# Kernel optimization log

Hardware: AMD Instinct MI355X
Metric: run time of the kernel (lower is better)

The kernel has to match this reference:

```python
import jax, jax.numpy as jnp
import numpy as np
from jax import lax

R = 0.1  # radius_graph radius (matches init kwarg r)


def setup_inputs() -> dict:
    key = jax.random.key(0)
    ks = jax.random.split(key, 16)
    B, O, K, F = 8, 4, 512, 3
    H = 128
    def lin(k, fan_in, fan_out):
        return jax.random.normal(k, (fan_in, fan_out), jnp.float32) / np.sqrt(fan_in)
    return {
        "points": jax.random.uniform(ks[0], (B, O, K, F), jnp.float32),
        "com": jax.random.normal(ks[1], (B, O, 3), jnp.float32),
        "com_vel": jax.random.normal(ks[2], (B, O, 3), jnp.float32),
        "angle": jax.random.normal(ks[3], (B, O, 3), jnp.float32),
        "angle_vel": jax.random.normal(ks[4], (B, O, 3), jnp.float32),
        "padding": jnp.ones((B, O, K), jnp.float32),
        "W0": lin(ks[5], 2 * F, H), "b0": jnp.zeros((H,), jnp.float32),
        "W1": lin(ks[6], H, H), "b1": jnp.zeros((H,), jnp.float32),
        "W2": lin(ks[7], H, H), "b2": jnp.zeros((H,), jnp.float32),
        "Wfc": lin(ks[8], H, 2 * F), "bfc": jnp.zeros((2 * F,), jnp.float32),
        "knn": 8,
        "pred_len": 10,
    }


def reference(points, com, com_vel, angle, angle_vel, padding,
              W0, b0, W1, b1, W2, b2, Wfc, bfc, knn, pred_len):
    B, O, K, F = points.shape
    N = O * K  # nodes per batch element
    pad = padding.reshape(B, N)                       # float mask [B,N]
    padb = pad > 0
    edge_ok = padb[:, :, None] & padb[:, None, :]     # valid src & dst
    not_self = ~jnp.eye(N, dtype=bool)
    eye = jnp.eye(N, dtype=points.dtype)

    states0 = jnp.concatenate([points, jnp.zeros_like(points)], -1).reshape(B, N, 2 * F)

    def gconv(a_hat, dinv, x, W, b):
        # GCNConv: out_i = sum_j A_hat[ij] d_i^-1/2 d_j^-1/2 (xW)_j + b
        h = (x @ W) * dinv[..., None]
        return jnp.einsum('bij,bjd->bid', a_hat, h) * dinv[..., None] + b

    def step(states, _):
        pos = states[..., :3]                         # [B,N,3]
        d2 = jnp.sum((pos[:, :, None, :] - pos[:, None, :, :]) ** 2, -1)
        adj = (d2 < R * R) & not_self & edge_ok       # radius_graph + padding mask
        a_hat = lax.stop_gradient(adj.astype(states.dtype) + eye)  # self-loops (all nodes)
        dinv = lax.rsqrt(a_hat.sum(-1))               # deg >= 1
        x = jax.nn.relu(gconv(a_hat, dinv, states, W0, b0))
        x = jax.nn.relu(gconv(a_hat, dinv, x, W1, b1))
        x = jax.nn.relu(gconv(a_hat, dinv, x, W2, b2))
        res = x @ Wfc + bfc
        new = states + res * pad[..., None]
        return new, new

    _, traj = lax.scan(step, states0, None, length=pred_len)
    traj = jnp.concatenate([states0[:, None], jnp.swapaxes(traj, 0, 1)], axis=1)
    return traj.reshape(B, pred_len + 1, O, K, 2 * F)[..., :3]
```

## Files before the change

### kernel.cpp

```cpp
#include <hip/hip_runtime.h>
#include <math.h>

#define BB 8
#define NN 2048
#define HH 128
#define NSEG 8
#define SEGJ 256
#define SEGCAP 12
#define MAXNBR (NSEG*SEGCAP)
#define PREDL 10
#define TSTRIDE (NN*3)
#define OUT_BSTRIDE ((PREDL+1)*NN*3)


__global__ __launch_bounds__(256) void k_init(const float* __restrict__ points,
                                              float* __restrict__ states,
                                              float* __restrict__ out) {
    int idx = blockIdx.x * 256 + threadIdx.x;
    if (idx >= BB * NN) return;
    int b = idx >> 11;
    int n = idx & 2047;
    float px = points[idx * 3 + 0];
    float py = points[idx * 3 + 1];
    float pz = points[idx * 3 + 2];
    float* s = states + (size_t)idx * 6;
    s[0] = px; s[1] = py; s[2] = pz; s[3] = 0.f; s[4] = 0.f; s[5] = 0.f;
    float* o = out + (size_t)b * OUT_BSTRIDE + n * 3;
    o[0] = px; o[1] = py; o[2] = pz;
}

__global__ __launch_bounds__(512, 2) void k_adj(const float* __restrict__ states,
                                                float* __restrict__ xs0,
                                                float* __restrict__ dinv,
                                                int* __restrict__ nbr,
                                                int* __restrict__ cntN) {
    const float R2c = 0.01f;
    int b = blockIdx.x & 7;
    int tile = blockIdx.x >> 3;
    __shared__ float4 pos[NN];
    __shared__ int degs[512];
    __shared__ unsigned short jb[512][SEGCAP];
    const float* sb = states + (size_t)b * NN * 6;
    for (int j = threadIdx.x; j < NN; j += 512) {
        const float* r = sb + j * 6;
        pos[j] = make_float4(r[0], r[1], r[2], 0.f);
    }
    __syncthreads();
    int node = threadIdx.x & 63;
    int seg  = threadIdx.x >> 6;
    int i = tile * 64 + node;
    int gi = b * NN + i;
    float4 pi = pos[i];
    int cnt = 0;
    int j0 = seg * SEGJ;
#pragma unroll 4
    for (int j = j0; j < j0 + SEGJ; ++j) {
        float4 pj = pos[j];
        float dx = pi.x - pj.x;
        float dy = pi.y - pj.y;
        float dz = pi.z - pj.z;
        float d2 = __fadd_rn(__fadd_rn(__fmul_rn(dx, dx), __fmul_rn(dy, dy)),
                             __fmul_rn(dz, dz));
        if (d2 < R2c && j != i) {
            if (cnt < SEGCAP) jb[threadIdx.x][cnt] = (unsigned short)j;
            cnt++;
        }
    }
    if (cnt > SEGCAP) cnt = SEGCAP;
    degs[threadIdx.x] = cnt;
    __syncthreads();
    int off = 0;
    for (int s = 0; s < seg; ++s) off += degs[s * 64 + node];
    int base = gi * MAXNBR + off;
    for (int k = 0; k < cnt; ++k) nbr[base + k] = (int)jb[threadIdx.x][k];
    if (seg == NSEG - 1) {
        int tot = off + cnt;
        cntN[gi] = tot;
        float di = (float)(1.0 / sqrt((double)(1 + tot)));
        dinv[gi] = di;
        const float* srow = sb + (size_t)i * 6;
        float* xr = xs0 + (size_t)gi * 6;
#pragma unroll
        for (int c = 0; c < 6; ++c) xr[c] = di * srow[c];
    }
}

__global__ __launch_bounds__(512, 4) void k_l0(const float* __restrict__ xs0,
                                               const float* __restrict__ dinv,
                                               const int* __restrict__ nbr,
                                               const int* __restrict__ cntN,
                                               const float* __restrict__ W0,
                                               const float* __restrict__ b0,
                                               float* __restrict__ xs1) {
    int b = blockIdx.x & 7;
    int tile = blockIdx.x >> 3;
    int node = threadIdx.x >> 4;
    int part = threadIdx.x & 15;
    int i = tile * 32 + node;
    int gi = b * NN + i;
    float g[6];
    {
        const float* sr = xs0 + (size_t)gi * 6;
        float2 a0 = *(const float2*)sr;
        float2 a1 = *(const float2*)(sr + 2);
        float2 a2 = *(const float2*)(sr + 4);
        g[0] = a0.x; g[1] = a0.y; g[2] = a1.x; g[3] = a1.y; g[4] = a2.x; g[5] = a2.y;
    }
    int cnt = cntN[gi];
    const int* nb = nbr + gi * MAXNBR;
    for (int k = 0; k < cnt; ++k) {
        int j = nb[k];
        const float* xr = xs0 + (size_t)(b * NN + j) * 6;
        float2 v0 = *(const float2*)xr;
        float2 v1 = *(const float2*)(xr + 2);
        float2 v2 = *(const float2*)(xr + 4);
        g[0] += v0.x; g[1] += v0.y; g[2] += v1.x;
        g[3] += v1.y; g[4] += v2.x; g[5] += v2.y;
    }
    float di = dinv[gi];
#pragma unroll
    for (int c = 0; c < 6; ++c) g[c] *= di;
    int c0 = part * 8;
    float y[8];
#pragma unroll
    for (int r = 0; r < 2; ++r) {
        float4 bv = *(const float4*)(b0 + c0 + r * 4);
        y[r * 4 + 0] = bv.x; y[r * 4 + 1] = bv.y; y[r * 4 + 2] = bv.z; y[r * 4 + 3] = bv.w;
    }
#pragma unroll
    for (int k = 0; k < 6; ++k) {
        float u = g[k];
        const float* wr = W0 + k * HH + c0;
#pragma unroll
        for (int r = 0; r < 2; ++r) {
            float4 w = *(const float4*)(wr + r * 4);
            y[r * 4 + 0] = fmaf(u, w.x, y[r * 4 + 0]);
            y[r * 4 + 1] = fmaf(u, w.y, y[r * 4 + 1]);
            y[r * 4 + 2] = fmaf(u, w.z, y[r * 4 + 2]);
            y[r * 4 + 3] = fmaf(u, w.w, y[r * 4 + 3]);
        }
    }
    float* xo = xs1 + (size_t)gi * HH + c0;
#pragma unroll
    for (int r = 0; r < 2; ++r) {
        float4 v;
        v.x = di * fmaxf(y[r * 4 + 0], 0.f);
        v.y = di * fmaxf(y[r * 4 + 1], 0.f);
        v.z = di * fmaxf(y[r * 4 + 2], 0.f);
        v.w = di * fmaxf(y[r * 4 + 3], 0.f);
        *(float4*)(xo + r * 4) = v;
    }
}

__device__ __forceinline__ void gather_into_lds(const float* __restrict__ xin,
                                                const float* __restrict__ dinv,
                                                const int* __restrict__ nbr,
                                                const int* __restrict__ cntN,
                                                int b, int tile,
                                                float (*uS)[HH + 4]) {
    const int node = threadIdx.x >> 4;
    const int part = threadIdx.x & 15;
    const int i = tile * 32 + node;
    const int gi = b * NN + i;
    const int c0 = part * 8;
    float acc[8];
    const float* xs = xin + (size_t)gi * HH + c0;
#pragma unroll
    for (int r = 0; r < 2; ++r) *(float4*)&acc[r * 4] = *(const float4*)(xs + r * 4);
    const int cnt = cntN[gi];
    const int* nb = nbr + gi * MAXNBR;
    for (int k = 0; k < cnt; ++k) {
        const int j = nb[k];
        const float* xr = xin + (size_t)(b * NN + j) * HH + c0;
#pragma unroll
        for (int r = 0; r < 2; ++r) {
            float v[4];
            *(float4*)v = *(const float4*)(xr + r * 4);
            acc[r * 4 + 0] += v[0]; acc[r * 4 + 1] += v[1];
            acc[r * 4 + 2] += v[2]; acc[r * 4 + 3] += v[3];
        }
    }
    const float di = dinv[gi];
#pragma unroll
    for (int r = 0; r < 2; ++r) {
        float4 o;
        o.x = acc[r * 4 + 0] * di; o.y = acc[r * 4 + 1] * di;
        o.z = acc[r * 4 + 2] * di; o.w = acc[r * 4 + 3] * di;
        *(float4*)&uS[node][c0 + r * 4] = o;
    }
}

__device__ __forceinline__ void gemm_panel1(const float (*uS)[HH + 4],
                                            const float* __restrict__ wbuf,
                                            int p, int node, int cA,
                                            float y0[8]) {
#pragma unroll 2
    for (int r = 0; r < 32; r += 4) {
        float ua[4];
        *(float4*)ua = *(const float4*)(&uS[node][p * 32 + r]);
        const float* wrow = wbuf + r * HH + cA;
#pragma unroll
        for (int q = 0; q < 4; ++q) {
            float4 wa = *(const float4*)(wrow + q * HH);
            float4 wb = *(const float4*)(wrow + q * HH + 64);
            float u0 = ua[q];
            y0[0] = fmaf(u0, wa.x, y0[0]); y0[1] = fmaf(u0, wa.y, y0[1]);
            y0[2] = fmaf(u0, wa.z, y0[2]); y0[3] = fmaf(u0, wa.w, y0[3]);
            y0[4] = fmaf(u0, wb.x, y0[4]); y0[5] = fmaf(u0, wb.y, y0[5]);
            y0[6] = fmaf(u0, wb.z, y0[6]); y0[7] = fmaf(u0, wb.w, y0[7]);
        }
    }
}

__global__ __launch_bounds__(512, 4) void k_mid(const float* __restrict__ xin,
                                                const float* __restrict__ dinv,
                                                const int* __restrict__ nbr,
                                                const int* __restrict__ cntN,
                                                const float* __restrict__ W,
                                                const float* __restrict__ bias,
                                                float* __restrict__ xout) {
    __shared__ __align__(16) float uS[32][HH + 4];
    __shared__ __align__(16) float wS[2][32 * HH];
    int b = blockIdx.x & 7;
    int tile = blockIdx.x >> 3;
    int t = threadIdx.x;
    const float4* Wf4 = (const float4*)W;
    float4 wreg[2];
    wreg[0] = Wf4[t]; wreg[1] = Wf4[t + 512];
    gather_into_lds(xin, dinv, nbr, cntN, b, tile, uS);
    {
        float4* ws4 = (float4*)wS[0];
        ws4[t] = wreg[0]; ws4[t + 512] = wreg[1];
    }
    __syncthreads();
    int cb = t & 15, node = t >> 4;
    int cA = cb * 4;
    float y0[8];
    {
        float4 bv0 = *(const float4*)(bias + cA);
        float4 bv1 = *(const float4*)(bias + cA + 64);
        y0[0] = bv0.x; y0[1] = bv0.y; y0[2] = bv0.z; y0[3] = bv0.w;
        y0[4] = bv1.x; y0[5] = bv1.y; y0[6] = bv1.z; y0[7] = bv1.w;
    }
#pragma unroll
    for (int p = 0; p < 4; ++p) {
        if (p < 3) {
            wreg[0] = Wf4[(p + 1) * 1024 + t];
            wreg[1] = Wf4[(p + 1) * 1024 + t + 512];
        }
        gemm_panel1(uS, wS[p & 1], p, node, cA, y0);
        if (p < 3) {
            float4* ws4 = (float4*)wS[1 - (p & 1)];
            ws4[t] = wreg[0]; ws4[t + 512] = wreg[1];
            __syncthreads();
        }
    }
    int g0 = b * NN + tile * 32 + node;
    float di0 = dinv[g0];
    float* o0 = xout + (size_t)g0 * HH + cA;
    float4 va, vb;
    va.x = di0 * fmaxf(y0[0], 0.f); va.y = di0 * fmaxf(y0[1], 0.f);
    va.z = di0 * fmaxf(y0[2], 0.f); va.w = di0 * fmaxf(y0[3], 0.f);
    vb.x = di0 * fmaxf(y0[4], 0.f); vb.y = di0 * fmaxf(y0[5], 0.f);
    vb.z = di0 * fmaxf(y0[6], 0.f); vb.w = di0 * fmaxf(y0[7], 0.f);
    *(float4*)o0 = va; *(float4*)(o0 + 64) = vb;
}

__global__ __launch_bounds__(512, 4) void k_last(const float* __restrict__ xin,
                                                 const float* __restrict__ dinv,
                                                 const int* __restrict__ nbr,
                                                 const int* __restrict__ cntN,
                                                 const float* __restrict__ W2,
                                                 const float* __restrict__ b2,
                                                 const float* __restrict__ Wfc,
                                                 const float* __restrict__ bfc,
                                                 const float* __restrict__ padding,
                                                 float* __restrict__ states,
                                                 float* __restrict__ outt) {
    __shared__ __align__(16) float uS[32][HH + 4];
    __shared__ __align__(16) float wS[2][32 * HH];
    int b = blockIdx.x & 7;
    int tile = blockIdx.x >> 3;
    int t = threadIdx.x;
    const float4* Wf4 = (const float4*)W2;
    float4 wreg[2];
    wreg[0] = Wf4[t]; wreg[1] = Wf4[t + 512];
    gather_into_lds(xin, dinv, nbr, cntN, b, tile, uS);
    {
        float4* ws4 = (float4*)wS[0];
        ws4[t] = wreg[0]; ws4[t + 512] = wreg[1];
    }
    __syncthreads();
    int cb = t & 15, node = t >> 4;
    int cA = cb * 4;
    float y0[8];
    {
        float4 bv0 = *(const float4*)(b2 + cA);
        float4 bv1 = *(const float4*)(b2 + cA + 64);
        y0[0] = bv0.x; y0[1] = bv0.y; y0[2] = bv0.z; y0[3] = bv0.w;
        y0[4] = bv1.x; y0[5] = bv1.y; y0[6] = bv1.z; y0[7] = bv1.w;
    }
#pragma unroll
    for (int p = 0; p < 4; ++p) {
        if (p < 3) {
            wreg[0] = Wf4[(p + 1) * 1024 + t];
            wreg[1] = Wf4[(p + 1) * 1024 + t + 512];
        }
        gemm_panel1(uS, wS[p & 1], p, node, cA, y0);
        if (p < 3) {
            float4* ws4 = (float4*)wS[1 - (p & 1)];
            ws4[t] = wreg[0]; ws4[t + 512] = wreg[1];
            __syncthreads();
        }
    }
    __syncthreads();
    float* y3  = wS[0];
    float* wfc = wS[1];
    for (int q = t; q < HH * 6; q += 512) wfc[q] = Wfc[q];
    {
        float4 v;
        v.x = fmaxf(y0[0], 0.f); v.y = fmaxf(y0[1], 0.f);
        v.z = fmaxf(y0[2], 0.f); v.w = fmaxf(y0[3], 0.f);
        *(float4*)&y3[node * HH + cA] = v;
        v.x = fmaxf(y0[4], 0.f); v.y = fmaxf(y0[5], 0.f);
        v.z = fmaxf(y0[6], 0.f); v.w = fmaxf(y0[7], 0.f);
        *(float4*)&y3[node * HH + cA + 64] = v;
    }
    __syncthreads();
    if (t < 192) {
        int n = t / 6;
        int c = t - n * 6;
        float r = bfc[c];
        for (int k = 0; k < HH; k += 4) {
            float yv[4];
            *(float4*)yv = *(const float4*)&y3[n * HH + k];
            r = fmaf(yv[0], wfc[(k + 0) * 6 + c], r);
            r = fmaf(yv[1], wfc[(k + 1) * 6 + c], r);
            r = fmaf(yv[2], wfc[(k + 2) * 6 + c], r);
            r = fmaf(yv[3], wfc[(k + 3) * 6 + c], r);
        }
        int i = tile * 32 + n;
        int gi = b * NN + i;
        float pv = padding[b * NN + i];
        float s = states[(size_t)gi * 6 + c] + r * pv;
        states[(size_t)gi * 6 + c] = s;
        if (c < 3) outt[(size_t)b * OUT_BSTRIDE + i * 3 + c] = s;
    }
}

extern "C" void kernel_launch(void* const* d_in, const int* in_sizes, int n_in,
                              void* d_out, int out_size, void* d_ws, size_t ws_size,
                              hipStream_t stream) {
    (void)in_sizes; (void)n_in; (void)out_size; (void)ws_size;
    const float* points  = (const float*)d_in[0];
    const float* padding = (const float*)d_in[5];
    const float* W0  = (const float*)d_in[6];
    const float* b0  = (const float*)d_in[7];
    const float* W1  = (const float*)d_in[8];
    const float* b1  = (const float*)d_in[9];
    const float* W2  = (const float*)d_in[10];
    const float* b2  = (const float*)d_in[11];
    const float* Wfc = (const float*)d_in[12];
    const float* bfc = (const float*)d_in[13];
    float* out = (float*)d_out;

    float* ws     = (float*)d_ws;
    float* states = ws;
    float* xs0    = states + BB * NN * 6;
    float* xs1    = xs0 + BB * NN * 6;
    float* xs2    = xs1 + BB * NN * HH;
    float* dinvp  = xs2 + BB * NN * HH;
    int*   nbr    = (int*)(dinvp + BB * NN);
    int*   cntN   = nbr + BB * NN * MAXNBR;

    k_init<<<(BB * NN) / 256, 256, 0, stream>>>(points, states, out);
    for (int t = 0; t < PREDL; ++t) {
        k_adj<<<256, 512, 0, stream>>>(states, xs0, dinvp, nbr, cntN);
        k_l0<<<512, 512, 0, stream>>>(xs0, dinvp, nbr, cntN, W0, b0, xs1);
        k_mid<<<512, 512, 0, stream>>>(xs1, dinvp, nbr, cntN, W1, b1, xs2);
        k_last<<<512, 512, 0, stream>>>(xs2, dinvp, nbr, cntN, W2, b2, Wfc, bfc,
                                        padding, states,
                                        out + (size_t)(t + 1) * TSTRIDE);
    }
}
```

Baseline: 778.7 us.

## Fold init into first adjacency pass and double threads per node in GCN layers

Removes the separate init kernel: on the first step the adjacency kernel reads positions straight from points and writes the initial states, output frame and scaled features itself. The layer kernels go from 512 to 1024 threads per block, 32 threads per node each handling 4 channels instead of 16 threads handling 8. This gives more parallelism for the neighbour-gather latency and fewer registers per thread. The cost is more blocks' worth of redundant gather index loads, and `__launch_bounds__(1024, 8)` asks for an occupancy that shared memory may not allow.

```diff
diff --git a/kernel.cpp b/kernel.cpp
--- a/kernel.cpp
+++ b/kernel.cpp
@@ -13,27 +13,14 @@
 #define OUT_BSTRIDE ((PREDL+1)*NN*3)
 
 
-__global__ __launch_bounds__(256) void k_init(const float* __restrict__ points,
-                                              float* __restrict__ states,
-                                              float* __restrict__ out) {
-    int idx = blockIdx.x * 256 + threadIdx.x;
-    if (idx >= BB * NN) return;
-    int b = idx >> 11;
-    int n = idx & 2047;
-    float px = points[idx * 3 + 0];
-    float py = points[idx * 3 + 1];
-    float pz = points[idx * 3 + 2];
-    float* s = states + (size_t)idx * 6;
-    s[0] = px; s[1] = py; s[2] = pz; s[3] = 0.f; s[4] = 0.f; s[5] = 0.f;
-    float* o = out + (size_t)b * OUT_BSTRIDE + n * 3;
-    o[0] = px; o[1] = py; o[2] = pz;
-}
-
-__global__ __launch_bounds__(512, 2) void k_adj(const float* __restrict__ states,
+__global__ __launch_bounds__(512, 2) void k_adj(float* __restrict__ states,
+                                                const float* __restrict__ points,
                                                 float* __restrict__ xs0,
                                                 float* __restrict__ dinv,
                                                 int* __restrict__ nbr,
-                                                int* __restrict__ cntN) {
+                                                int* __restrict__ cntN,
+                                                float* __restrict__ out,
+                                                int first) {
     const float R2c = 0.01f;
     int b = blockIdx.x & 7;
     int tile = blockIdx.x >> 3;
@@ -41,9 +28,17 @@
     __shared__ int degs[512];
     __shared__ unsigned short jb[512][SEGCAP];
     const float* sb = states + (size_t)b * NN * 6;
-    for (int j = threadIdx.x; j < NN; j += 512) {
-        const float* r = sb + j * 6;
-        pos[j] = make_float4(r[0], r[1], r[2], 0.f);
+    if (first) {
+        const float* pb = points + (size_t)b * NN * 3;
+        for (int j = threadIdx.x; j < NN; j += 512) {
+            const float* r = pb + j * 3;
+            pos[j] = make_float4(r[0], r[1], r[2], 0.f);
+        }
+    } else {
+        for (int j = threadIdx.x; j < NN; j += 512) {
+            const float* r = sb + j * 6;
+            pos[j] = make_float4(r[0], r[1], r[2], 0.f);
+        }
     }
     __syncthreads();
     int node = threadIdx.x & 63;
@@ -78,24 +73,34 @@
         cntN[gi] = tot;
         float di = (float)(1.0 / sqrt((double)(1 + tot)));
         dinv[gi] = di;
-        const float* srow = sb + (size_t)i * 6;
         float* xr = xs0 + (size_t)gi * 6;
-#pragma unroll
-        for (int c = 0; c < 6; ++c) xr[c] = di * srow[c];
-    }
-}
-
-__global__ __launch_bounds__(512, 4) void k_l0(const float* __restrict__ xs0,
-                                               const float* __restrict__ dinv,
-                                               const int* __restrict__ nbr,
-                                               const int* __restrict__ cntN,
-                                               const float* __restrict__ W0,
-                                               const float* __restrict__ b0,
-                                               float* __restrict__ xs1) {
+        if (first) {
+            float px = pi.x, py = pi.y, pz = pi.z;
+            float* s = states + (size_t)gi * 6;
+            s[0] = px; s[1] = py; s[2] = pz; s[3] = 0.f; s[4] = 0.f; s[5] = 0.f;
+            float* o = out + (size_t)b * OUT_BSTRIDE + i * 3;
+            o[0] = px; o[1] = py; o[2] = pz;
+            xr[0] = di * px; xr[1] = di * py; xr[2] = di * pz;
+            xr[3] = 0.f; xr[4] = 0.f; xr[5] = 0.f;
+        } else {
+            const float* srow = sb + (size_t)i * 6;
+#pragma unroll
+            for (int c = 0; c < 6; ++c) xr[c] = di * srow[c];
+        }
+    }
+}
+
+__global__ __launch_bounds__(1024, 8) void k_l0(const float* __restrict__ xs0,
+                                                const float* __restrict__ dinv,
+                                                const int* __restrict__ nbr,
+                                                const int* __restrict__ cntN,
+                                                const float* __restrict__ W0,
+                                                const float* __restrict__ b0,
+                                                float* __restrict__ xs1) {
     int b = blockIdx.x & 7;
     int tile = blockIdx.x >> 3;
-    int node = threadIdx.x >> 4;
-    int part = threadIdx.x & 15;
+    int node = threadIdx.x >> 5;
+    int part = threadIdx.x & 31;
     int i = tile * 32 + node;
     int gi = b * NN + i;
     float g[6];
@@ -120,36 +125,28 @@
     float di = dinv[gi];
 #pragma unroll
     for (int c = 0; c < 6; ++c) g[c] *= di;
-    int c0 = part * 8;
-    float y[8];
-#pragma unroll
-    for (int r = 0; r < 2; ++r) {
-        float4 bv = *(const float4*)(b0 + c0 + r * 4);
-        y[r * 4 + 0] = bv.x; y[r * 4 + 1] = bv.y; y[r * 4 + 2] = bv.z; y[r * 4 + 3] = bv.w;
+    int c0 = part * 4;
+    float y[4];
+    {
+        float4 bv = *(const float4*)(b0 + c0);
+        y[0] = bv.x; y[1] = bv.y; y[2] = bv.z; y[3] = bv.w;
     }
 #pragma unroll
     for (int k = 0; k < 6; ++k) {
         float u = g[k];
-        const float* wr = W0 + k * HH + c0;
-#pragma unroll
-        for (int r = 0; r < 2; ++r) {
-            float4 w = *(const float4*)(wr + r * 4);
-            y[r * 4 + 0] = fmaf(u, w.x, y[r * 4 + 0]);
-            y[r * 4 + 1] = fmaf(u, w.y, y[r * 4 + 1]);
-            y[r * 4 + 2] = fmaf(u, w.z, y[r * 4 + 2]);
-            y[r * 4 + 3] = fmaf(u, w.w, y[r * 4 + 3]);
-        }
+        float4 w = *(const float4*)(W0 + k * HH + c0);
+        y[0] = fmaf(u, w.x, y[0]);
+        y[1] = fmaf(u, w.y, y[1]);
+        y[2] = fmaf(u, w.z, y[2]);
+        y[3] = fmaf(u, w.w, y[3]);
     }
     float* xo = xs1 + (size_t)gi * HH + c0;
-#pragma unroll
-    for (int r = 0; r < 2; ++r) {
-        float4 v;
-        v.x = di * fmaxf(y[r * 4 + 0], 0.f);
-        v.y = di * fmaxf(y[r * 4 + 1], 0.f);
-        v.z = di * fmaxf(y[r * 4 + 2], 0.f);
-        v.w = di * fmaxf(y[r * 4 + 3], 0.f);
-        *(float4*)(xo + r * 4) = v;
-    }
+    float4 v;
+    v.x = di * fmaxf(y[0], 0.f);
+    v.y = di * fmaxf(y[1], 0.f);
+    v.z = di * fmaxf(y[2], 0.f);
+    v.w = di * fmaxf(y[3], 0.f);
+    *(float4*)xo = v;
 }
 
 __device__ __forceinline__ void gather_into_lds(const float* __restrict__ xin,
@@ -158,42 +155,31 @@
                                                 const int* __restrict__ cntN,
                                                 int b, int tile,
                                                 float (*uS)[HH + 4]) {
-    const int node = threadIdx.x >> 4;
-    const int part = threadIdx.x & 15;
+    const int node = threadIdx.x >> 5;
+    const int part = threadIdx.x & 31;
     const int i = tile * 32 + node;
     const int gi = b * NN + i;
-    const int c0 = part * 8;
-    float acc[8];
-    const float* xs = xin + (size_t)gi * HH + c0;
-#pragma unroll
-    for (int r = 0; r < 2; ++r) *(float4*)&acc[r * 4] = *(const float4*)(xs + r * 4);
+    const int c0 = part * 4;
+    float acc[4];
+    *(float4*)acc = *(const float4*)(xin + (size_t)gi * HH + c0);
     const int cnt = cntN[gi];
     const int* nb = nbr + gi * MAXNBR;
     for (int k = 0; k < cnt; ++k) {
         const int j = nb[k];
-        const float* xr = xin + (size_t)(b * NN + j) * HH + c0;
-#pragma unroll
-        for (int r = 0; r < 2; ++r) {
-            float v[4];
-            *(float4*)v = *(const float4*)(xr + r * 4);
-            acc[r * 4 + 0] += v[0]; acc[r * 4 + 1] += v[1];
-            acc[r * 4 + 2] += v[2]; acc[r * 4 + 3] += v[3];
-        }
+        float v[4];
+        *(float4*)v = *(const float4*)(xin + (size_t)(b * NN + j) * HH + c0);
+        acc[0] += v[0]; acc[1] += v[1]; acc[2] += v[2]; acc[3] += v[3];
     }
     const float di = dinv[gi];
-#pragma unroll
-    for (int r = 0; r < 2; ++r) {
-        float4 o;
-        o.x = acc[r * 4 + 0] * di; o.y = acc[r * 4 + 1] * di;
-        o.z = acc[r * 4 + 2] * di; o.w = acc[r * 4 + 3] * di;
-        *(float4*)&uS[node][c0 + r * 4] = o;
-    }
+    float4 o;
+    o.x = acc[0] * di; o.y = acc[1] * di; o.z = acc[2] * di; o.w = acc[3] * di;
+    *(float4*)&uS[node][c0] = o;
 }
 
 __device__ __forceinline__ void gemm_panel1(const float (*uS)[HH + 4],
                                             const float* __restrict__ wbuf,
                                             int p, int node, int cA,
-                                            float y0[8]) {
+                                            float y0[4]) {
 #pragma unroll 2
     for (int r = 0; r < 32; r += 4) {
         float ua[4];
@@ -202,129 +188,103 @@
 #pragma unroll
         for (int q = 0; q < 4; ++q) {
             float4 wa = *(const float4*)(wrow + q * HH);
-            float4 wb = *(const float4*)(wrow + q * HH + 64);
             float u0 = ua[q];
-            y0[0] = fmaf(u0, wa.x, y0[0]); y0[1] = fmaf(u0, wa.y, y0[1]);
-            y0[2] = fmaf(u0, wa.z, y0[2]); y0[3] = fmaf(u0, wa.w, y0[3]);
-            y0[4] = fmaf(u0, wb.x, y0[4]); y0[5] = fmaf(u0, wb.y, y0[5]);
-            y0[6] = fmaf(u0, wb.z, y0[6]); y0[7] = fmaf(u0, wb.w, y0[7]);
-        }
-    }
-}
-
-__global__ __launch_bounds__(512, 4) void k_mid(const float* __restrict__ xin,
-                                                const float* __restrict__ dinv,
-                                                const int* __restrict__ nbr,
-                                                const int* __restrict__ cntN,
-                                                const float* __restrict__ W,
-                                                const float* __restrict__ bias,
-                                                float* __restrict__ xout) {
+            y0[0] = fmaf(u0, wa.x, y0[0]);
+            y0[1] = fmaf(u0, wa.y, y0[1]);
+            y0[2] = fmaf(u0, wa.z, y0[2]);
+            y0[3] = fmaf(u0, wa.w, y0[3]);
+        }
+    }
+}
+
+__global__ __launch_bounds__(1024, 8) void k_mid(const float* __restrict__ xin,
+                                                 const float* __restrict__ dinv,
+                                                 const int* __restrict__ nbr,
+                                                 const int* __restrict__ cntN,
+                                                 const float* __restrict__ W,
+                                                 const float* __restrict__ bias,
+                                                 float* __restrict__ xout) {
     __shared__ __align__(16) float uS[32][HH + 4];
     __shared__ __align__(16) float wS[2][32 * HH];
     int b = blockIdx.x & 7;
     int tile = blockIdx.x >> 3;
     int t = threadIdx.x;
     const float4* Wf4 = (const float4*)W;
-    float4 wreg[2];
-    wreg[0] = Wf4[t]; wreg[1] = Wf4[t + 512];
+    float4 wreg = Wf4[t];
     gather_into_lds(xin, dinv, nbr, cntN, b, tile, uS);
-    {
-        float4* ws4 = (float4*)wS[0];
-        ws4[t] = wreg[0]; ws4[t + 512] = wreg[1];
-    }
-    __syncthreads();
-    int cb = t & 15, node = t >> 4;
+    ((float4*)wS[0])[t] = wreg;
+    __syncthreads();
+    int cb = t & 31, node = t >> 5;
     int cA = cb * 4;
-    float y0[8];
-    {
-        float4 bv0 = *(const float4*)(bias + cA);
-        float4 bv1 = *(const float4*)(bias + cA + 64);
-        y0[0] = bv0.x; y0[1] = bv0.y; y0[2] = bv0.z; y0[3] = bv0.w;
-        y0[4] = bv1.x; y0[5] = bv1.y; y0[6] = bv1.z; y0[7] = bv1.w;
+    float y0[4];
+    {
+        float4 bv = *(const float4*)(bias + cA);
+        y0[0] = bv.x; y0[1] = bv.y; y0[2] = bv.z; y0[3] = bv.w;
     }
 #pragma unroll
     for (int p = 0; p < 4; ++p) {
-        if (p < 3) {
-            wreg[0] = Wf4[(p + 1) * 1024 + t];
-            wreg[1] = Wf4[(p + 1) * 1024 + t + 512];
-        }
+        if (p < 3) wreg = Wf4[(p + 1) * 1024 + t];
         gemm_panel1(uS, wS[p & 1], p, node, cA, y0);
         if (p < 3) {
-            float4* ws4 = (float4*)wS[1 - (p & 1)];
-            ws4[t] = wreg[0]; ws4[t + 512] = wreg[1];
+            ((float4*)wS[1 - (p & 1)])[t] = wreg;
             __syncthreads();
         }
     }
     int g0 = b * NN + tile * 32 + node;
     float di0 = dinv[g0];
     float* o0 = xout + (size_t)g0 * HH + cA;
-    float4 va, vb;
+    float4 va;
     va.x = di0 * fmaxf(y0[0], 0.f); va.y = di0 * fmaxf(y0[1], 0.f);
     va.z = di0 * fmaxf(y0[2], 0.f); va.w = di0 * fmaxf(y0[3], 0.f);
-    vb.x = di0 * fmaxf(y0[4], 0.f); vb.y = di0 * fmaxf(y0[5], 0.f);
-    vb.z = di0 * fmaxf(y0[6], 0.f); vb.w = di0 * fmaxf(y0[7], 0.f);
-    *(float4*)o0 = va; *(float4*)(o0 + 64) = vb;
-}
-
-__global__ __launch_bounds__(512, 4) void k_last(const float* __restrict__ xin,
-                                                 const float* __restrict__ dinv,
-                                                 const int* __restrict__ nbr,
-                                                 const int* __restrict__ cntN,
-                                                 const float* __restrict__ W2,
-                                                 const float* __restrict__ b2,
-                                                 const float* __restrict__ Wfc,
-                                                 const float* __restrict__ bfc,
-                                                 const float* __restrict__ padding,
-                                                 float* __restrict__ states,
-                                                 float* __restrict__ outt) {
+    *(float4*)o0 = va;
+}
+
+__global__ __launch_bounds__(1024, 8) void k_last(const float* __restrict__ xin,
+                                                  const float* __restrict__ dinv,
+                                                  const int* __restrict__ nbr,
+                                                  const int* __restrict__ cntN,
+                                                  const float* __restrict__ W2,
+                                                  const float* __restrict__ b2,
+                                                  const float* __restrict__ Wfc,
+                                                  const float* __restrict__ bfc,
+                                                  const float* __restrict__ padding,
+                                                  float* __restrict__ states,
+                                                  float* __restrict__ outt) {
     __shared__ __align__(16) float uS[32][HH + 4];
     __shared__ __align__(16) float wS[2][32 * HH];
     int b = blockIdx.x & 7;
     int tile = blockIdx.x >> 3;
     int t = threadIdx.x;
     const float4* Wf4 = (const float4*)W2;
-    float4 wreg[2];
-    wreg[0] = Wf4[t]; wreg[1] = Wf4[t + 512];
+    float4 wreg = Wf4[t];
     gather_into_lds(xin, dinv, nbr, cntN, b, tile, uS);
-    {
-        float4* ws4 = (float4*)wS[0];
-        ws4[t] = wreg[0]; ws4[t + 512] = wreg[1];
-    }
-    __syncthreads();
-    int cb = t & 15, node = t >> 4;
+    ((float4*)wS[0])[t] = wreg;
+    __syncthreads();
+    int cb = t & 31, node = t >> 5;
     int cA = cb * 4;
-    float y0[8];
-    {
-        float4 bv0 = *(const float4*)(b2 + cA);
-        float4 bv1 = *(const float4*)(b2 + cA + 64);
-        y0[0] = bv0.x; y0[1] = bv0.y; y0[2] = bv0.z; y0[3] = bv0.w;
-        y0[4] = bv1.x; y0[5] = bv1.y; y0[6] = bv1.z; y0[7] = bv1.w;
+    float y0[4];
+    {
+        float4 bv = *(const float4*)(b2 + cA);
+        y0[0] = bv.x; y0[1] = bv.y; y0[2] = bv.z; y0[3] = bv.w;
     }
 #pragma unroll
     for (int p = 0; p < 4; ++p) {
-        if (p < 3) {
-            wreg[0] = Wf4[(p + 1) * 1024 + t];
-            wreg[1] = Wf4[(p + 1) * 1024 + t + 512];
-        }
+        if (p < 3) wreg = Wf4[(p + 1) * 1024 + t];
         gemm_panel1(uS, wS[p & 1], p, node, cA, y0);
         if (p < 3) {
-            float4* ws4 = (float4*)wS[1 - (p & 1)];
-            ws4[t] = wreg[0]; ws4[t + 512] = wreg[1];
+            ((float4*)wS[1 - (p & 1)])[t] = wreg;
             __syncthreads();
         }
     }
     __syncthreads();
     float* y3  = wS[0];
     float* wfc = wS[1];
-    for (int q = t; q < HH * 6; q += 512) wfc[q] = Wfc[q];
+    for (int q = t; q < HH * 6; q += 1024) wfc[q] = Wfc[q];
     {
         float4 v;
         v.x = fmaxf(y0[0], 0.f); v.y = fmaxf(y0[1], 0.f);
         v.z = fmaxf(y0[2], 0.f); v.w = fmaxf(y0[3], 0.f);
         *(float4*)&y3[node * HH + cA] = v;
-        v.x = fmaxf(y0[4], 0.f); v.y = fmaxf(y0[5], 0.f);
-        v.z = fmaxf(y0[6], 0.f); v.w = fmaxf(y0[7], 0.f);
-        *(float4*)&y3[node * HH + cA + 64] = v;
     }
     __syncthreads();
     if (t < 192) {
@@ -373,13 +333,13 @@
     int*   nbr    = (int*)(dinvp + BB * NN);
     int*   cntN   = nbr + BB * NN * MAXNBR;
 
-    k_init<<<(BB * NN) / 256, 256, 0, stream>>>(points, states, out);
     for (int t = 0; t < PREDL; ++t) {
-        k_adj<<<256, 512, 0, stream>>>(states, xs0, dinvp, nbr, cntN);
-        k_l0<<<512, 512, 0, stream>>>(xs0, dinvp, nbr, cntN, W0, b0, xs1);
-        k_mid<<<512, 512, 0, stream>>>(xs1, dinvp, nbr, cntN, W1, b1, xs2);
-        k_last<<<512, 512, 0, stream>>>(xs2, dinvp, nbr, cntN, W2, b2, Wfc, bfc,
-                                        padding, states,
-                                        out + (size_t)(t + 1) * TSTRIDE);
-    }
-}
+        k_adj<<<256, 512, 0, stream>>>(states, points, xs0, dinvp, nbr, cntN,
+                                       out, (t == 0) ? 1 : 0);
+        k_l0<<<512, 1024, 0, stream>>>(xs0, dinvp, nbr, cntN, W0, b0, xs1);
+        k_mid<<<512, 1024, 0, stream>>>(xs1, dinvp, nbr, cntN, W1, b1, xs2);
+        k_last<<<512, 1024, 0, stream>>>(xs2, dinvp, nbr, cntN, W2, b2, Wfc, bfc,
+                                         padding, states,
+                                         out + (size_t)(t + 1) * TSTRIDE);
+    }
+}
```

Result: no change. 786.5 us (+1.0%).
